# Kernel tuning notes

Measured on AMD Instinct MI355X. Metric: run time of the kernel, lower is better.

The kernel has to match this reference:

```python
import jax, jax.numpy as jnp
import numpy as np
import math

HIDDEN = 512
NUM_HEADS = 16
HEAD_DIM = HIDDEN // NUM_HEADS          # 32
SPOW_DIM = HEAD_DIM * (HEAD_DIM + 1) // 2  # 528
GAMMA = 0.9
B, S = 2, 1024

_TRIU_I, _TRIU_J = np.triu_indices(HEAD_DIM, k=1)
_SQRT2 = math.sqrt(2.0)


def spow2(x):
    # x: (..., d) -> (..., d*(d+1)//2); squares then sqrt(2)*upper-tri cross terms
    squares = x * x
    cross = _SQRT2 * (x[..., _TRIU_I] * x[..., _TRIU_J])
    return jnp.concatenate([squares, cross], axis=-1)


def setup_inputs() -> dict:
    key = jax.random.key(0)
    ks = jax.random.split(key, 9)
    lim = 1.0 / math.sqrt(HIDDEN)
    w = lambda k: jax.random.uniform(k, (HIDDEN, HIDDEN), jnp.float32, -lim, lim)
    b = lambda k: jax.random.uniform(k, (HIDDEN,), jnp.float32, -lim, lim)
    return {
        "x": jax.random.normal(ks[0], (B, S, HIDDEN), jnp.float32),
        "q_w": w(ks[1]), "q_b": b(ks[2]),
        "k_w": w(ks[3]), "k_b": b(ks[4]),
        "v_w": w(ks[5]), "v_b": b(ks[6]),
        "o_w": w(ks[7]), "o_b": b(ks[8]),
    }


def reference(x, q_w, q_b, k_w, k_b, v_w, v_b, o_w, o_b):
    Bb, Ss, Hh = x.shape
    q = (x @ q_w + q_b).reshape(Bb, Ss, NUM_HEADS, HEAD_DIM)
    k = (x @ k_w + k_b).reshape(Bb, Ss, NUM_HEADS, HEAD_DIM)
    v = (x @ v_w + v_b).reshape(Bb, Ss, NUM_HEADS, HEAD_DIM)

    sq = spow2(q)  # [B,S,H,Dspow]
    sk = spow2(k)  # [B,S,H,Dspow]

    # time-major for scan
    sq_t = jnp.moveaxis(sq, 1, 0)  # [S,B,H,D]
    sk_t = jnp.moveaxis(sk, 1, 0)
    v_t = jnp.moveaxis(v, 1, 0)    # [S,B,H,hd]

    state0 = jnp.zeros((Bb, NUM_HEADS, SPOW_DIM, HEAD_DIM), x.dtype)

    def step(state, inp):
        skt, sqt, vt = inp
        # state = gamma*state + spow_k \otimes v  -> [B,H,Dspow,hd]
        state = GAMMA * state + skt[..., :, None] * vt[..., None, :]
        out = jnp.einsum('bhD,bhDd->bhd', sqt, state)
        return state, out

    _, outs = jax.lax.scan(step, state0, (sk_t, sq_t, v_t))  # [S,B,H,hd]
    out = jnp.moveaxis(outs, 0, 1).reshape(Bb, Ss, Hh)
    return out @ o_w + o_b
```

## Files before the change

### kernel.cpp

```cpp
#include <hip/hip_runtime.h>
#include <hip/hip_bf16.h>
#include <math.h>

#define HIDDEN 512
#define NHEADS 16
#define HDIM   32
#define BATCH  2
#define SEQ    1024
#define MROWS  (BATCH * SEQ)

constexpr float LOG2_GAMMA = -0.15200309344504997f;

typedef __hip_bfloat16 bf16;
typedef __attribute__((ext_vector_type(8))) short short8;
typedef __attribute__((ext_vector_type(4))) float f32x4;

__device__ __forceinline__ void async16(const void* g, void* l) {
    __builtin_amdgcn_global_load_lds(
        (const __attribute__((address_space(1))) void*)g,
        (__attribute__((address_space(3))) void*)l, 16, 0, 0);
}

__device__ __forceinline__ unsigned short f2bf_bits(float f) {
    bf16 b = __float2bfloat16(f);
    return *(unsigned short*)&b;
}

__global__ __launch_bounds__(256) void prep(
    const float* __restrict__ x,
    const float* __restrict__ qw, const float* __restrict__ kw,
    const float* __restrict__ vw, const float* __restrict__ ow,
    bf16* __restrict__ xb, bf16* __restrict__ wqkvt, bf16* __restrict__ wot)
{
    const int blk = blockIdx.x, tid = threadIdx.x;
    if (blk < 256) {
        const int widx = blk >> 6;
        const int tile = blk & 63;
        const int tk = (tile & 7) * 64, tn = (tile >> 3) * 64;
        const float* w = widx == 0 ? qw : widx == 1 ? kw : widx == 2 ? vw : ow;
        __shared__ float t[64][65];
        #pragma unroll
        for (int u = 0; u < 4; ++u) {
            const int r = u * 16 + (tid >> 4);
            const int c = (tid & 15) * 4;
            float4 v = *(const float4*)&w[(size_t)(tk + r) * 512 + tn + c];
            t[r][c + 0] = v.x; t[r][c + 1] = v.y; t[r][c + 2] = v.z; t[r][c + 3] = v.w;
        }
        __syncthreads();
        #pragma unroll
        for (int u = 0; u < 2; ++u) {
            const int rr = u * 32 + (tid >> 3);
            const int cc = (tid & 7) * 8;
            alignas(16) unsigned short tmp[8];
            #pragma unroll
            for (int i = 0; i < 8; ++i) tmp[i] = f2bf_bits(t[cc + i][rr]);
            bf16* dst = (widx < 3)
                ? &wqkvt[((size_t)widx * 512 + tn + rr) * 512 + tk + cc]
                : &wot[(size_t)(tn + rr) * 512 + tk + cc];
            *(short8*)dst = *(short8*)tmp;
        }
    } else {
        #pragma unroll
        for (int u = 0; u < 4; ++u) {
            const int idx = (blk - 256) * 1024 + u * 256 + tid;
            float4 v = ((const float4*)x)[idx];
            unsigned pk0 = (unsigned)f2bf_bits(v.x) | ((unsigned)f2bf_bits(v.y) << 16);
            unsigned pk1 = (unsigned)f2bf_bits(v.z) | ((unsigned)f2bf_bits(v.w) << 16);
            uint2 pk = {pk0, pk1};
            *(uint2*)&xb[(size_t)idx * 4] = pk;
        }
    }
}

template<int MS, int EPI>
__global__ __launch_bounds__(256) void gemm_persistB(
    const bf16* __restrict__ A, const bf16* __restrict__ Bt,
    const float* __restrict__ b0, const float* __restrict__ b1,
    const float* __restrict__ b2,
    float* __restrict__ Cf, bf16* __restrict__ Cb, int ldc)
{
    constexpr int K = 512;
    constexpr int LDB = 520;
    constexpr int TM = MS / 64;
    __shared__ alignas(16) short Bs[64 * LDB];

    const int tid = threadIdx.x;
    const int wave = tid >> 6, lane = tid & 63;
    const int fr = lane & 15, quad = lane >> 4;
    const int n0 = blockIdx.x * 64;
    const int m0 = blockIdx.y * MS;

    #pragma unroll
    for (int i = 0; i < 16; ++i) {
        const int row = wave * 16 + i;
        async16(&Bt[(size_t)(n0 + row) * K + lane * 8], &Bs[row * LDB]);
    }
    __syncthreads();

    const bf16* pa = &A[(size_t)(m0 + wave * (MS / 4) + fr) * K + quad * 8];

    f32x4 acc[TM][4] = {};
    #pragma unroll
    for (int ks = 0; ks < 16; ++ks) {
        short8 bfrag[4];
        #pragma unroll
        for (int j = 0; j < 4; ++j)
            bfrag[j] = *(const short8*)&Bs[(j * 16 + fr) * LDB + ks * 32 + quad * 8];
        #pragma unroll
        for (int i = 0; i < TM; ++i) {
            short8 af = *(const short8*)(pa + (size_t)i * 16 * K + ks * 32);
            #pragma unroll
            for (int j = 0; j < 4; ++j)
                acc[i][j] = __builtin_amdgcn_mfma_f32_16x16x32_bf16(
                    af, bfrag[j], acc[i][j], 0, 0, 0);
        }
    }

    if (EPI == 1) {
        const int seg = n0 >> 9;
        const float* bp = seg == 0 ? b0 : seg == 1 ? b1 : b2;
        const float sgn = seg == 0 ? 0.5f : seg == 1 ? -0.5f : 0.0f;
        #pragma unroll
        for (int i = 0; i < TM; ++i) {
            const int mrow = m0 + wave * (MS / 4) + i * 16 + quad * 4;
            float sc[4];
            #pragma unroll
            for (int r = 0; r < 4; ++r)
                sc[r] = exp2f((float)((mrow + r) & 63) * (sgn * LOG2_GAMMA));
            #pragma unroll
            for (int j = 0; j < 4; ++j) {
                const int n = n0 + j * 16 + fr;
                const float bv = bp[n & 511];
                #pragma unroll
                for (int r = 0; r < 4; ++r) {
                    unsigned short h = f2bf_bits((acc[i][j][r] + bv) * sc[r]);
                    *(unsigned short*)&Cb[(size_t)(mrow + r) * ldc + n] = h;
                }
            }
        }
    } else {
        #pragma unroll
        for (int i = 0; i < TM; ++i) {
            const int mrow = m0 + wave * (MS / 4) + i * 16 + quad * 4;
            #pragma unroll
            for (int j = 0; j < 4; ++j) {
                const int n = n0 + j * 16 + fr;
                const float bv = b0[n];
                #pragma unroll
                for (int r = 0; r < 4; ++r)
                    Cf[(size_t)(mrow + r) * ldc + n] = acc[i][j][r] + bv;
            }
        }
    }
}

__global__ __launch_bounds__(256) void power_attn_mfma(
    const bf16* __restrict__ qkv, bf16* __restrict__ atc)
{
    __shared__ alignas(16) short Qs[64 * 32];
    __shared__ alignas(16) short Ks[64 * 32];
    __shared__ alignas(16) short Vt[32 * 80];
    __shared__ alignas(16) short Ps[64 * 72];

    const int tid = threadIdx.x, wave = tid >> 6, lane = tid & 63;
    const int chunk = blockIdx.x, bh = blockIdx.y;
    const int b = bh >> 4, h = bh & 15;
    const int mb = b * SEQ + chunk * 64;
    const int fr = lane & 15, quad = lane >> 4;

    async16(&qkv[(size_t)(mb + wave * 16 + (lane >> 2)) * 1536 + h * 32 + (lane & 3) * 8],
            &Qs[wave * 512]);

    f32x4 o0 = {}, o1 = {};
    const int jstart = chunk >= 2 ? chunk - 2 : 0;

    for (int j = jstart; j <= chunk; ++j) {
        __syncthreads();
        const int sb = b * SEQ + j * 64;
        async16(&qkv[(size_t)(sb + wave * 16 + (lane >> 2)) * 1536 + 512 + h * 32 + (lane & 3) * 8],
                &Ks[wave * 512]);
        if (tid < 128) {
            const int p = tid >> 2, s = p * 2, dbase = (tid & 3) * 8;
            const short* g = (const short*)&qkv[(size_t)(sb + s) * 1536 + 1024 + h * 32 + dbase];
            short8 v0 = *(const short8*)g;
            short8 v1 = *(const short8*)(g + 1536);
            #pragma unroll
            for (int i = 0; i < 8; ++i) {
                unsigned pk = (unsigned)(unsigned short)v0[i]
                            | ((unsigned)(unsigned short)v1[i] << 16);
                *(unsigned*)&Vt[(dbase + i) * 80 + s] = pk;
            }
        }
        __syncthreads();

        short8 aq = *(const short8*)&Qs[(wave * 16 + fr) * 32 + quad * 8];
        f32x4 sAcc[4] = {};
        #pragma unroll
        for (int nt = 0; nt < 4; ++nt) {
            short8 bk = *(const short8*)&Ks[(nt * 16 + fr) * 32 + quad * 8];
            sAcc[nt] = __builtin_amdgcn_mfma_f32_16x16x32_bf16(aq, bk, sAcc[nt], 0, 0, 0);
        }

        const int dj = chunk - j;
        const float sj = exp2f(64.0f * (float)dj * LOG2_GAMMA);
        const int tbase = wave * 16 + quad * 4;
        #pragma unroll
        for (int nt = 0; nt < 4; ++nt) {
            const int s_l = nt * 16 + fr;
            #pragma unroll
            for (int r = 0; r < 4; ++r) {
                const int t_l = tbase + r;
                float pv = sAcc[nt][r];
                pv = pv * pv * sj;
                if (dj == 0 && s_l > t_l) pv = 0.0f;
                Ps[t_l * 72 + s_l] = (short)f2bf_bits(pv);
            }
        }
        short8 a0 = *(const short8*)&Ps[(wave * 16 + fr) * 72 + quad * 8];
        short8 a1 = *(const short8*)&Ps[(wave * 16 + fr) * 72 + 32 + quad * 8];
        short8 b00 = *(const short8*)&Vt[fr * 80 + quad * 8];
        short8 b01 = *(const short8*)&Vt[fr * 80 + 32 + quad * 8];
        short8 b10 = *(const short8*)&Vt[(16 + fr) * 80 + quad * 8];
        short8 b11 = *(const short8*)&Vt[(16 + fr) * 80 + 32 + quad * 8];
        o0 = __builtin_amdgcn_mfma_f32_16x16x32_bf16(a0, b00, o0, 0, 0, 0);
        o0 = __builtin_amdgcn_mfma_f32_16x16x32_bf16(a1, b01, o0, 0, 0, 0);
        o1 = __builtin_amdgcn_mfma_f32_16x16x32_bf16(a0, b10, o1, 0, 0, 0);
        o1 = __builtin_amdgcn_mfma_f32_16x16x32_bf16(a1, b11, o1, 0, 0, 0);
    }

    #pragma unroll
    for (int r = 0; r < 4; ++r) {
        const size_t row = mb + wave * 16 + quad * 4 + r;
        const int col = h * 32 + fr;
        *(unsigned short*)&atc[row * 512 + col]      = f2bf_bits(o0[r]);
        *(unsigned short*)&atc[row * 512 + col + 16] = f2bf_bits(o1[r]);
    }
}

extern "C" void kernel_launch(void* const* d_in, const int* in_sizes, int n_in,
                              void* d_out, int out_size, void* d_ws, size_t ws_size,
                              hipStream_t stream)
{
    const float* x  = (const float*)d_in[0];
    const float* qw = (const float*)d_in[1];
    const float* qb = (const float*)d_in[2];
    const float* kw = (const float*)d_in[3];
    const float* kb = (const float*)d_in[4];
    const float* vw = (const float*)d_in[5];
    const float* vb = (const float*)d_in[6];
    const float* ow = (const float*)d_in[7];
    const float* ob = (const float*)d_in[8];
    float* out = (float*)d_out;

    char* w = (char*)d_ws;
    bf16* xb    = (bf16*)(w);
    bf16* wqkvt = (bf16*)(w + (2ull  << 20));
    bf16* wot   = (bf16*)(w + (2ull  << 20) + (1536ull << 10));
    bf16* qkvb  = (bf16*)(w + (4ull  << 20));
    bf16* atc   = (bf16*)(w + (10ull << 20));

    prep<<<512, 256, 0, stream>>>(x, qw, kw, vw, ow, xb, wqkvt, wot);

    gemm_persistB<128, 1><<<dim3(1536 / 64, MROWS / 128), 256, 0, stream>>>(
        xb, wqkvt, qb, kb, vb, nullptr, qkvb, 1536);

    power_attn_mfma<<<dim3(SEQ / 64, BATCH * NHEADS), 256, 0, stream>>>(qkvb, atc);

    gemm_persistB<64, 0><<<dim3(512 / 64, MROWS / 64), 256, 0, stream>>>(
        atc, wot, ob, nullptr, nullptr, out, nullptr, 512);
}
```

Measured before the change: 97.72 us.

## Fuse x bf16 conversion into QKV GEMM and preload all K/V chunks

```diff
diff --git a/kernel.cpp b/kernel.cpp
--- a/kernel.cpp
+++ b/kernel.cpp
@@ -26,55 +26,42 @@
     return *(unsigned short*)&b;
 }
 
-__global__ __launch_bounds__(256) void prep(
-    const float* __restrict__ x,
+__global__ __launch_bounds__(256) void prep_w(
     const float* __restrict__ qw, const float* __restrict__ kw,
     const float* __restrict__ vw, const float* __restrict__ ow,
-    bf16* __restrict__ xb, bf16* __restrict__ wqkvt, bf16* __restrict__ wot)
+    bf16* __restrict__ wqkvt, bf16* __restrict__ wot)
 {
     const int blk = blockIdx.x, tid = threadIdx.x;
-    if (blk < 256) {
-        const int widx = blk >> 6;
-        const int tile = blk & 63;
-        const int tk = (tile & 7) * 64, tn = (tile >> 3) * 64;
-        const float* w = widx == 0 ? qw : widx == 1 ? kw : widx == 2 ? vw : ow;
-        __shared__ float t[64][65];
-        #pragma unroll
-        for (int u = 0; u < 4; ++u) {
-            const int r = u * 16 + (tid >> 4);
-            const int c = (tid & 15) * 4;
-            float4 v = *(const float4*)&w[(size_t)(tk + r) * 512 + tn + c];
-            t[r][c + 0] = v.x; t[r][c + 1] = v.y; t[r][c + 2] = v.z; t[r][c + 3] = v.w;
-        }
-        __syncthreads();
-        #pragma unroll
-        for (int u = 0; u < 2; ++u) {
-            const int rr = u * 32 + (tid >> 3);
-            const int cc = (tid & 7) * 8;
-            alignas(16) unsigned short tmp[8];
-            #pragma unroll
-            for (int i = 0; i < 8; ++i) tmp[i] = f2bf_bits(t[cc + i][rr]);
-            bf16* dst = (widx < 3)
-                ? &wqkvt[((size_t)widx * 512 + tn + rr) * 512 + tk + cc]
-                : &wot[(size_t)(tn + rr) * 512 + tk + cc];
-            *(short8*)dst = *(short8*)tmp;
-        }
-    } else {
-        #pragma unroll
-        for (int u = 0; u < 4; ++u) {
-            const int idx = (blk - 256) * 1024 + u * 256 + tid;
-            float4 v = ((const float4*)x)[idx];
-            unsigned pk0 = (unsigned)f2bf_bits(v.x) | ((unsigned)f2bf_bits(v.y) << 16);
-            unsigned pk1 = (unsigned)f2bf_bits(v.z) | ((unsigned)f2bf_bits(v.w) << 16);
-            uint2 pk = {pk0, pk1};
-            *(uint2*)&xb[(size_t)idx * 4] = pk;
-        }
-    }
-}
-
-template<int MS, int EPI>
+    const int widx = blk >> 6;
+    const int tile = blk & 63;
+    const int tk = (tile & 7) * 64, tn = (tile >> 3) * 64;
+    const float* w = widx == 0 ? qw : widx == 1 ? kw : widx == 2 ? vw : ow;
+    __shared__ float t[64][65];
+    #pragma unroll
+    for (int u = 0; u < 4; ++u) {
+        const int r = u * 16 + (tid >> 4);
+        const int c = (tid & 15) * 4;
+        float4 v = *(const float4*)&w[(size_t)(tk + r) * 512 + tn + c];
+        t[r][c + 0] = v.x; t[r][c + 1] = v.y; t[r][c + 2] = v.z; t[r][c + 3] = v.w;
+    }
+    __syncthreads();
+    #pragma unroll
+    for (int u = 0; u < 2; ++u) {
+        const int rr = u * 32 + (tid >> 3);
+        const int cc = (tid & 7) * 8;
+        alignas(16) unsigned short tmp[8];
+        #pragma unroll
+        for (int i = 0; i < 8; ++i) tmp[i] = f2bf_bits(t[cc + i][rr]);
+        bf16* dst = (widx < 3)
+            ? &wqkvt[((size_t)widx * 512 + tn + rr) * 512 + tk + cc]
+            : &wot[(size_t)(tn + rr) * 512 + tk + cc];
+        *(short8*)dst = *(short8*)tmp;
+    }
+}
+
+template<int MS, int EPI, bool AF32>
 __global__ __launch_bounds__(256) void gemm_persistB(
-    const bf16* __restrict__ A, const bf16* __restrict__ Bt,
+    const void* __restrict__ Av, const bf16* __restrict__ Bt,
     const float* __restrict__ b0, const float* __restrict__ b1,
     const float* __restrict__ b2,
     float* __restrict__ Cf, bf16* __restrict__ Cb, int ldc)
@@ -97,7 +84,7 @@
     }
     __syncthreads();
 
-    const bf16* pa = &A[(size_t)(m0 + wave * (MS / 4) + fr) * K + quad * 8];
+    const int arow = m0 + wave * (MS / 4) + fr;
 
     f32x4 acc[TM][4] = {};
     #pragma unroll
@@ -108,7 +95,20 @@
             bfrag[j] = *(const short8*)&Bs[(j * 16 + fr) * LDB + ks * 32 + quad * 8];
         #pragma unroll
         for (int i = 0; i < TM; ++i) {
-            short8 af = *(const short8*)(pa + (size_t)i * 16 * K + ks * 32);
+            short8 af;
+            if (AF32) {
+                const float* pa = (const float*)Av
+                    + (size_t)(arow + i * 16) * K + quad * 8 + ks * 32;
+                float4 u0 = *(const float4*)pa;
+                float4 u1 = *(const float4*)(pa + 4);
+                alignas(16) unsigned short tmp[8] = {
+                    f2bf_bits(u0.x), f2bf_bits(u0.y), f2bf_bits(u0.z), f2bf_bits(u0.w),
+                    f2bf_bits(u1.x), f2bf_bits(u1.y), f2bf_bits(u1.z), f2bf_bits(u1.w)};
+                af = *(const short8*)tmp;
+            } else {
+                af = *(const short8*)((const bf16*)Av
+                    + (size_t)(arow + i * 16) * K + quad * 8 + ks * 32);
+            }
             #pragma unroll
             for (int j = 0; j < 4; ++j)
                 acc[i][j] = __builtin_amdgcn_mfma_f32_16x16x32_bf16(
@@ -158,8 +158,8 @@
     const bf16* __restrict__ qkv, bf16* __restrict__ atc)
 {
     __shared__ alignas(16) short Qs[64 * 32];
-    __shared__ alignas(16) short Ks[64 * 32];
-    __shared__ alignas(16) short Vt[32 * 80];
+    __shared__ alignas(16) short Ks[3][64 * 32];
+    __shared__ alignas(16) short Vt[3][32 * 80];
     __shared__ alignas(16) short Ps[64 * 72];
 
     const int tid = threadIdx.x, wave = tid >> 6, lane = tid & 63;
@@ -167,20 +167,23 @@
     const int b = bh >> 4, h = bh & 15;
     const int mb = b * SEQ + chunk * 64;
     const int fr = lane & 15, quad = lane >> 4;
+    const int jstart = chunk >= 2 ? chunk - 2 : 0;
+    const int cnt = chunk - jstart + 1;
 
     async16(&qkv[(size_t)(mb + wave * 16 + (lane >> 2)) * 1536 + h * 32 + (lane & 3) * 8],
             &Qs[wave * 512]);
-
-    f32x4 o0 = {}, o1 = {};
-    const int jstart = chunk >= 2 ? chunk - 2 : 0;
-
-    for (int j = jstart; j <= chunk; ++j) {
-        __syncthreads();
-        const int sb = b * SEQ + j * 64;
+    for (int jj = 0; jj < cnt; ++jj) {
+        const int sb = b * SEQ + (jstart + jj) * 64;
         async16(&qkv[(size_t)(sb + wave * 16 + (lane >> 2)) * 1536 + 512 + h * 32 + (lane & 3) * 8],
-                &Ks[wave * 512]);
-        if (tid < 128) {
-            const int p = tid >> 2, s = p * 2, dbase = (tid & 3) * 8;
+                &Ks[jj][wave * 512]);
+    }
+    #pragma unroll
+    for (int u = 0; u < 2; ++u) {
+        const int task = tid + u * 256;
+        if (task < cnt * 128) {
+            const int jj = task >> 7, tt = task & 127;
+            const int s = (tt >> 2) * 2, dbase = (tt & 3) * 8;
+            const int sb = b * SEQ + (jstart + jj) * 64;
             const short* g = (const short*)&qkv[(size_t)(sb + s) * 1536 + 1024 + h * 32 + dbase];
             short8 v0 = *(const short8*)g;
             short8 v1 = *(const short8*)(g + 1536);
@@ -188,20 +191,24 @@
             for (int i = 0; i < 8; ++i) {
                 unsigned pk = (unsigned)(unsigned short)v0[i]
                             | ((unsigned)(unsigned short)v1[i] << 16);
-                *(unsigned*)&Vt[(dbase + i) * 80 + s] = pk;
-            }
-        }
-        __syncthreads();
-
-        short8 aq = *(const short8*)&Qs[(wave * 16 + fr) * 32 + quad * 8];
+                *(unsigned*)&Vt[jj][(dbase + i) * 80 + s] = pk;
+            }
+        }
+    }
+    __syncthreads();
+
+    short8 aq = *(const short8*)&Qs[(wave * 16 + fr) * 32 + quad * 8];
+    f32x4 o0 = {}, o1 = {};
+
+    for (int jj = 0; jj < cnt; ++jj) {
         f32x4 sAcc[4] = {};
         #pragma unroll
         for (int nt = 0; nt < 4; ++nt) {
-            short8 bk = *(const short8*)&Ks[(nt * 16 + fr) * 32 + quad * 8];
+            short8 bk = *(const short8*)&Ks[jj][(nt * 16 + fr) * 32 + quad * 8];
             sAcc[nt] = __builtin_amdgcn_mfma_f32_16x16x32_bf16(aq, bk, sAcc[nt], 0, 0, 0);
         }
 
-        const int dj = chunk - j;
+        const int dj = cnt - 1 - jj;
         const float sj = exp2f(64.0f * (float)dj * LOG2_GAMMA);
         const int tbase = wave * 16 + quad * 4;
         #pragma unroll
@@ -218,10 +225,10 @@
         }
         short8 a0 = *(const short8*)&Ps[(wave * 16 + fr) * 72 + quad * 8];
         short8 a1 = *(const short8*)&Ps[(wave * 16 + fr) * 72 + 32 + quad * 8];
-        short8 b00 = *(const short8*)&Vt[fr * 80 + quad * 8];
-        short8 b01 = *(const short8*)&Vt[fr * 80 + 32 + quad * 8];
-        short8 b10 = *(const short8*)&Vt[(16 + fr) * 80 + quad * 8];
-        short8 b11 = *(const short8*)&Vt[(16 + fr) * 80 + 32 + quad * 8];
+        short8 b00 = *(const short8*)&Vt[jj][fr * 80 + quad * 8];
+        short8 b01 = *(const short8*)&Vt[jj][fr * 80 + 32 + quad * 8];
+        short8 b10 = *(const short8*)&Vt[jj][(16 + fr) * 80 + quad * 8];
+        short8 b11 = *(const short8*)&Vt[jj][(16 + fr) * 80 + 32 + quad * 8];
         o0 = __builtin_amdgcn_mfma_f32_16x16x32_bf16(a0, b00, o0, 0, 0, 0);
         o0 = __builtin_amdgcn_mfma_f32_16x16x32_bf16(a1, b01, o0, 0, 0, 0);
         o1 = __builtin_amdgcn_mfma_f32_16x16x32_bf16(a0, b10, o1, 0, 0, 0);
@@ -253,19 +260,18 @@
     float* out = (float*)d_out;
 
     char* w = (char*)d_ws;
-    bf16* xb    = (bf16*)(w);
-    bf16* wqkvt = (bf16*)(w + (2ull  << 20));
-    bf16* wot   = (bf16*)(w + (2ull  << 20) + (1536ull << 10));
-    bf16* qkvb  = (bf16*)(w + (4ull  << 20));
-    bf16* atc   = (bf16*)(w + (10ull << 20));
-
-    prep<<<512, 256, 0, stream>>>(x, qw, kw, vw, ow, xb, wqkvt, wot);
-
-    gemm_persistB<128, 1><<<dim3(1536 / 64, MROWS / 128), 256, 0, stream>>>(
-        xb, wqkvt, qb, kb, vb, nullptr, qkvb, 1536);
+    bf16* wqkvt = (bf16*)(w);
+    bf16* wot   = (bf16*)(w + (1536ull << 10));
+    bf16* qkvb  = (bf16*)(w + (2ull << 20));
+    bf16* atc   = (bf16*)(w + (8ull << 20));
+
+    prep_w<<<256, 256, 0, stream>>>(qw, kw, vw, ow, wqkvt, wot);
+
+    gemm_persistB<128, 1, true><<<dim3(1536 / 64, MROWS / 128), 256, 0, stream>>>(
+        x, wqkvt, qb, kb, vb, nullptr, qkvb, 1536);
 
     power_attn_mfma<<<dim3(SEQ / 64, BATCH * NHEADS), 256, 0, stream>>>(qkvb, atc);
 
-    gemm_persistB<64, 0><<<dim3(512 / 64, MROWS / 64), 256, 0, stream>>>(
+    gemm_persistB<64, 0, false><<<dim3(512 / 64, MROWS / 64), 256, 0, stream>>>(
         atc, wot, ob, nullptr, nullptr, out, nullptr, 512);
 }
```

Measured after the change: 105.4 us. 7.8% more time.
